# Optimization experiments

Hardware: AMD Instinct MI355X
Metric: run time of the kernel (lower is better)

The kernel has to match this reference:

```python
import jax, jax.numpy as jnp
import numpy as np

D_MODEL = 1024
K_QUERY = 32
K_TOPK = 4

def setup_inputs() -> dict:
    key = jax.random.key(0)
    k1, k2, k3, k4, k5 = jax.random.split(key, 5)
    x = jax.random.normal(k1, (4, 2048, D_MODEL), dtype=jnp.float32)
    # nn.Linear(d_model, k_query): weight [k_query, d_model], bias [k_query]
    sc = 1.0 / np.sqrt(D_MODEL)
    Wq = jax.random.uniform(k2, (K_QUERY, D_MODEL), jnp.float32, -sc, sc)
    bq = jax.random.uniform(k3, (K_QUERY,), jnp.float32, -sc, sc)
    Wk = jax.random.uniform(k4, (K_QUERY, D_MODEL), jnp.float32, -sc, sc)
    bk = jax.random.uniform(k5, (K_QUERY,), jnp.float32, -sc, sc)
    return {"x": x, "Wq": Wq, "bq": bq, "Wk": Wk, "bk": bk}

def reference(x, Wq, bq, Wk, bk):
    # x: [B, T, D]
    queries = jnp.einsum('btd,kd->btk', x, Wq) + bq      # [B, T, Kq]
    keys = jnp.einsum('btd,kd->btk', x, Wk) + bk         # [B, T, Kq]
    sim = jnp.einsum('btk,bsk->bts', queries, keys)      # [B, T, T]
    sim = sim / jnp.sqrt(jnp.float32(queries.shape[-1]))
    _, topk_idx = jax.lax.top_k(sim, K_TOPK)              # [B, T, K]
    # gather neighbors per (b, t): x[b, topk_idx[b, t]] -> [B, T, K, D]
    neighbors = jax.vmap(lambda xb, ib: xb[ib])(x, topk_idx)
    gathered = neighbors.mean(axis=2)                     # [B, T, D]
    return gathered
```

## Files before the change

kernel.cpp:

```cpp
#include <hip/hip_runtime.h>
#include <math.h>

#define D_MODEL 1024
#define T_SEQ   2048
#define NBATCH  4
#define NROWS   (NBATCH * T_SEQ)
#define NOUT    64
#define DCHUNK  256
#define NCHUNK  4

#define SKLD 264
#define SQLD 20

__device__ __forceinline__ bool key_gt(float av, int ai, float bv, int bi) {
    return (av > bv) || (av == bv && ai < bi);
}

__device__ __forceinline__ void cmpswap(float& v0, int& i0, float& v1, int& i1) {
    bool sw = key_gt(v1, i1, v0, i0);
    float nv0 = sw ? v1 : v0, nv1 = sw ? v0 : v1;
    int   ni0 = sw ? i1 : i0, ni1 = sw ? i0 : i1;
    v0 = nv0; v1 = nv1; i0 = ni0; i1 = ni1;
}

__device__ __forceinline__ void merge4(float (&a)[4], int (&ai)[4],
                                       float b0, int j0, float b1, int j1,
                                       float b2, int j2, float b3, int j3) {
    if (!key_gt(a[0], ai[0], b3, j3)) { a[0] = b3; ai[0] = j3; }
    if (!key_gt(a[1], ai[1], b2, j2)) { a[1] = b2; ai[1] = j2; }
    if (!key_gt(a[2], ai[2], b1, j1)) { a[2] = b1; ai[2] = j1; }
    if (!key_gt(a[3], ai[3], b0, j0)) { a[3] = b0; ai[3] = j0; }
    cmpswap(a[0], ai[0], a[2], ai[2]);
    cmpswap(a[1], ai[1], a[3], ai[3]);
    cmpswap(a[0], ai[0], a[1], ai[1]);
    cmpswap(a[2], ai[2], a[3], ai[3]);
}

__device__ __forceinline__ void insert4(float (&tv)[4], int (&tix)[4], float v, int idx) {
    if (v > tv[3]) {
        bool g0 = v > tv[0], g1 = v > tv[1], g2 = v > tv[2];
        float n0 = g0 ? v : tv[0];
        int   m0 = g0 ? idx : tix[0];
        float n1 = g1 ? (g0 ? tv[0] : v) : tv[1];
        int   m1 = g1 ? (g0 ? tix[0] : idx) : tix[1];
        float n2 = g2 ? (g1 ? tv[1] : v) : tv[2];
        int   m2 = g2 ? (g1 ? tix[1] : idx) : tix[2];
        float n3 = g2 ? tv[2] : v;
        int   m3 = g2 ? tix[2] : idx;
        tv[0] = n0; tv[1] = n1; tv[2] = n2; tv[3] = n3;
        tix[0] = m0; tix[1] = m1; tix[2] = m2; tix[3] = m3;
    }
}

__global__ __launch_bounds__(256) void wprep_kernel(
    const float* __restrict__ Wq, const float* __restrict__ Wk,
    double* __restrict__ Wdt)
{
    const int idx = blockIdx.x * 256 + threadIdx.x;
    const int o = idx & 63;
    const int d = idx >> 6;
    float v = (o < 32) ? Wq[(size_t)o * D_MODEL + d]
                       : Wk[(size_t)(o - 32) * D_MODEL + d];
    Wdt[(size_t)d * 64 + o] = (double)v;
}

__global__ __launch_bounds__(256) void proj_partial(
    const float* __restrict__ x, const double* __restrict__ Wdt,
    double* __restrict__ part )
{
    const int rl = threadIdx.x & 63;
    const int og = __builtin_amdgcn_readfirstlane(threadIdx.x >> 6);
    const int rb = blockIdx.x & 127;
    const int c  = blockIdx.x >> 7;
    const int row = rb * 64 + rl;
    const int d0  = c * DCHUNK;

    const float4* xr = reinterpret_cast<const float4*>(x + (size_t)row * D_MODEL + d0);
    const double* wbase = Wdt + (size_t)d0 * 64 + og * 16;

    double acc[16];
    #pragma unroll
    for (int j = 0; j < 16; ++j) acc[j] = 0.0;

    #pragma unroll 2
    for (int i = 0; i < DCHUNK / 4; ++i) {
        float4 xv = xr[i];
        double xd[4] = {xv.x, xv.y, xv.z, xv.w};
        #pragma unroll
        for (int u = 0; u < 4; ++u) {
            const double* w = wbase + (size_t)(i * 4 + u) * 64;
            #pragma unroll
            for (int j = 0; j < 16; ++j)
                acc[j] = fma(xd[u], w[j], acc[j]);
        }
    }

    double* p = part + ((size_t)c * NOUT + og * 16) * NROWS + row;
    #pragma unroll
    for (int j = 0; j < 16; ++j)
        p[(size_t)j * NROWS] = acc[j];
}

__global__ __launch_bounds__(256) void proj_combine(
    const double* __restrict__ part,
    const float* __restrict__ bq, const float* __restrict__ bk,
    float* __restrict__ Qt, float* __restrict__ Kt)
{
    const int idx = blockIdx.x * 256 + threadIdx.x;
    const int out = idx >> 13;
    const int row = idx & (NROWS - 1);
    double s = 0.0;
    #pragma unroll
    for (int c = 0; c < NCHUNK; ++c)
        s += part[((size_t)c * NOUT + out) * NROWS + row];
    const int b = row >> 11, t = row & 2047;
    if (out < 32) {
        Qt[((size_t)b * 32 + out) * T_SEQ + t] = (float)(s + (double)bq[out]);
    } else {
        Kt[((size_t)b * 32 + (out - 32)) * T_SEQ + t] = (float)(s + (double)bk[out - 32]);
    }
}

__global__ __launch_bounds__(256) void topk_gather_kernel(
    const float* __restrict__ x, const float* __restrict__ Qt,
    const float* __restrict__ Kt, float* __restrict__ out)
{
    __shared__ float klds[32 * SKLD];
    __shared__ float qlds[32 * SQLD];
    __shared__ float candV[4][16][4];
    __shared__ int   candI[4][16][4];
    __shared__ int   topIdx[16][4];

    const int tid  = threadIdx.x;
    const int lane = tid & 63;
    const int wav  = tid >> 6;
    const int b    = blockIdx.x >> 7;
    const int tblk = (blockIdx.x & 127) * 16;

    const float* QtB = Qt + (size_t)b * 32 * T_SEQ;
    const float* KtB = Kt + (size_t)b * 32 * T_SEQ;

    if (tid < 128) {
        const int i  = tid >> 2;
        const int t4 = (tid & 3) * 4;
        float4 v = *reinterpret_cast<const float4*>(QtB + (size_t)i * T_SEQ + tblk + t4);
        *reinterpret_cast<float4*>(&qlds[i * SQLD + t4]) = v;
    }

    const int tg = tid & 3;
    const int t0 = tg * 4;
    const int s0 = (tid >> 2) * 4;

    float tv[4][4]; int tix[4][4];
    #pragma unroll
    for (int r = 0; r < 4; ++r)
        #pragma unroll
        for (int j = 0; j < 4; ++j) { tv[r][j] = -INFINITY; tix[r][j] = 0x7fffffff; }

    for (int st = 0; st < 8; ++st) {
        __syncthreads();
        #pragma unroll
        for (int j = 0; j < 8; ++j) {
            const int f  = (tid + j * 256) * 4;
            const int ki = f >> 8;
            const int ks = f & 255;
            float4 v = *reinterpret_cast<const float4*>(KtB + (size_t)ki * T_SEQ + st * 256 + ks);
            *reinterpret_cast<float4*>(&klds[ki * SKLD + ks]) = v;
        }
        __syncthreads();

        float acc[4][4];
        #pragma unroll
        for (int r = 0; r < 4; ++r)
            #pragma unroll
            for (int c = 0; c < 4; ++c) acc[r][c] = 0.f;

        #pragma unroll 8
        for (int i = 0; i < 32; ++i) {
            float4 qv = *reinterpret_cast<const float4*>(&qlds[i * SQLD + t0]);
            float4 kv = *reinterpret_cast<const float4*>(&klds[i * SKLD + s0]);
            const float qa[4] = {qv.x, qv.y, qv.z, qv.w};
            const float ka[4] = {kv.x, kv.y, kv.z, kv.w};
            #pragma unroll
            for (int r = 0; r < 4; ++r)
                #pragma unroll
                for (int c = 0; c < 4; ++c)
                    acc[r][c] = fmaf(qa[r], ka[c], acc[r][c]);
        }

        const int sbase = st * 256 + s0;
        #pragma unroll
        for (int c = 0; c < 4; ++c)
            #pragma unroll
            for (int r = 0; r < 4; ++r)
                insert4(tv[r], tix[r], acc[r][c], sbase + c);
    }

    #pragma unroll
    for (int m = 4; m <= 32; m <<= 1) {
        #pragma unroll
        for (int r = 0; r < 4; ++r) {
            float b0 = __shfl_xor(tv[r][0], m, 64);
            float b1 = __shfl_xor(tv[r][1], m, 64);
            float b2 = __shfl_xor(tv[r][2], m, 64);
            float b3 = __shfl_xor(tv[r][3], m, 64);
            int   j0 = __shfl_xor(tix[r][0], m, 64);
            int   j1 = __shfl_xor(tix[r][1], m, 64);
            int   j2 = __shfl_xor(tix[r][2], m, 64);
            int   j3 = __shfl_xor(tix[r][3], m, 64);
            merge4(tv[r], tix[r], b0, j0, b1, j1, b2, j2, b3, j3);
        }
    }

    if (lane < 4) {
        #pragma unroll
        for (int r = 0; r < 4; ++r)
            #pragma unroll
            for (int j = 0; j < 4; ++j) {
                candV[wav][lane * 4 + r][j] = tv[r][j];
                candI[wav][lane * 4 + r][j] = tix[r][j];
            }
    }
    __syncthreads();

    if (tid < 16) {
        float mv[4]; int mi[4];
        #pragma unroll
        for (int j = 0; j < 4; ++j) { mv[j] = candV[0][tid][j]; mi[j] = candI[0][tid][j]; }
        #pragma unroll
        for (int w = 1; w < 4; ++w)
            merge4(mv, mi,
                   candV[w][tid][0], candI[w][tid][0],
                   candV[w][tid][1], candI[w][tid][1],
                   candV[w][tid][2], candI[w][tid][2],
                   candV[w][tid][3], candI[w][tid][3]);
        #pragma unroll
        for (int j = 0; j < 4; ++j) topIdx[tid][j] = mi[j];
    }
    __syncthreads();

    const float* xb = x + (size_t)b * T_SEQ * D_MODEL;
    float* ob = out + ((size_t)b * T_SEQ + tblk) * D_MODEL;
    for (int r = 0; r < 16; ++r) {
        const int i0 = topIdx[r][0], i1 = topIdx[r][1], i2 = topIdx[r][2], i3 = topIdx[r][3];
        float4 a0 = *(reinterpret_cast<const float4*>(xb + (size_t)i0 * D_MODEL) + tid);
        float4 a1 = *(reinterpret_cast<const float4*>(xb + (size_t)i1 * D_MODEL) + tid);
        float4 a2 = *(reinterpret_cast<const float4*>(xb + (size_t)i2 * D_MODEL) + tid);
        float4 a3 = *(reinterpret_cast<const float4*>(xb + (size_t)i3 * D_MODEL) + tid);
        float4 o;
        o.x = (a0.x + a1.x + a2.x + a3.x) * 0.25f;
        o.y = (a0.y + a1.y + a2.y + a3.y) * 0.25f;
        o.z = (a0.z + a1.z + a2.z + a3.z) * 0.25f;
        o.w = (a0.w + a1.w + a2.w + a3.w) * 0.25f;
        *(reinterpret_cast<float4*>(ob + (size_t)r * D_MODEL) + tid) = o;
    }
}

extern "C" void kernel_launch(void* const* d_in, const int* in_sizes, int n_in,
                              void* d_out, int out_size, void* d_ws, size_t ws_size,
                              hipStream_t stream) {
    const float* x  = (const float*)d_in[0];
    const float* Wq = (const float*)d_in[1];
    const float* bq = (const float*)d_in[2];
    const float* Wk = (const float*)d_in[3];
    const float* bk = (const float*)d_in[4];
    float* out = (float*)d_out;

    char* wsb = (char*)d_ws;
    double* Wdt  = (double*)wsb;
    float*  Qt   = (float*)(wsb + (size_t)D_MODEL * NOUT * 8);
    float*  Kt   = Qt + (size_t)NBATCH * 32 * T_SEQ;
    double* part = (double*)(wsb + (size_t)D_MODEL * NOUT * 8
                                 + 2 * (size_t)NBATCH * 32 * T_SEQ * 4);

    wprep_kernel<<<dim3(256), dim3(256), 0, stream>>>(Wq, Wk, Wdt);
    proj_partial<<<dim3(NCHUNK * 128), dim3(256), 0, stream>>>(x, Wdt, part);
    proj_combine<<<dim3(NOUT * NROWS / 256), dim3(256), 0, stream>>>(part, bq, bk, Qt, Kt);
    topk_gather_kernel<<<dim3(512), dim3(256), 0, stream>>>(x, Qt, Kt, out);
}
```

Baseline: 179.7 us.

## Split similarity top-k across key halves and separate gather into merge kernel

The fused top-k/gather kernel is split into two kernels. The first computes similarity and a partial top-4 over half of the key sequence per block, using 128 threads with 4x8 register tiles, which doubles the block count. The second merges the two partial candidate lists and gathers/averages rows of x, 8 rows per block. The projection kernel also now uses 512 threads, each computing 8 outputs instead of 16. This adds an extra launch and a global round trip for the candidates in exchange for more parallelism and lower register pressure.

```diff
diff --git a/kernel.cpp b/kernel.cpp
--- a/kernel.cpp
+++ b/kernel.cpp
@@ -64,7 +64,7 @@
     Wdt[(size_t)d * 64 + o] = (double)v;
 }
 
-__global__ __launch_bounds__(256) void proj_partial(
+__global__ __launch_bounds__(512) void proj_partial(
     const float* __restrict__ x, const double* __restrict__ Wdt,
     double* __restrict__ part )
 {
@@ -76,13 +76,13 @@
     const int d0  = c * DCHUNK;
 
     const float4* xr = reinterpret_cast<const float4*>(x + (size_t)row * D_MODEL + d0);
-    const double* wbase = Wdt + (size_t)d0 * 64 + og * 16;
-
-    double acc[16];
-    #pragma unroll
-    for (int j = 0; j < 16; ++j) acc[j] = 0.0;
-
-    #pragma unroll 2
+    const double* wbase = Wdt + (size_t)d0 * 64 + og * 8;
+
+    double acc[8];
+    #pragma unroll
+    for (int j = 0; j < 8; ++j) acc[j] = 0.0;
+
+    #pragma unroll 4
     for (int i = 0; i < DCHUNK / 4; ++i) {
         float4 xv = xr[i];
         double xd[4] = {xv.x, xv.y, xv.z, xv.w};
@@ -90,14 +90,14 @@
         for (int u = 0; u < 4; ++u) {
             const double* w = wbase + (size_t)(i * 4 + u) * 64;
             #pragma unroll
-            for (int j = 0; j < 16; ++j)
+            for (int j = 0; j < 8; ++j)
                 acc[j] = fma(xd[u], w[j], acc[j]);
         }
     }
 
-    double* p = part + ((size_t)c * NOUT + og * 16) * NROWS + row;
-    #pragma unroll
-    for (int j = 0; j < 16; ++j)
+    double* p = part + ((size_t)c * NOUT + og * 8) * NROWS + row;
+    #pragma unroll
+    for (int j = 0; j < 8; ++j)
         p[(size_t)j * NROWS] = acc[j];
 }
 
@@ -121,26 +121,29 @@
     }
 }
 
-__global__ __launch_bounds__(256) void topk_gather_kernel(
-    const float* __restrict__ x, const float* __restrict__ Qt,
-    const float* __restrict__ Kt, float* __restrict__ out)
+__global__ __launch_bounds__(128) void sim_topk(
+    const float* __restrict__ Qt, const float* __restrict__ Kt,
+    float* __restrict__ candVal ,
+    int*   __restrict__ candIdx )
 {
     __shared__ float klds[32 * SKLD];
     __shared__ float qlds[32 * SQLD];
-    __shared__ float candV[4][16][4];
-    __shared__ int   candI[4][16][4];
-    __shared__ int   topIdx[16][4];
+    __shared__ float cV[2][16][4];
+    __shared__ int   cI[2][16][4];
 
     const int tid  = threadIdx.x;
     const int lane = tid & 63;
     const int wav  = tid >> 6;
-    const int b    = blockIdx.x >> 7;
-    const int tblk = (blockIdx.x & 127) * 16;
+    const int half = blockIdx.x & 1;
+    const int tt   = (blockIdx.x >> 1) & 127;
+    const int b    = blockIdx.x >> 8;
+    const int tblk = tt * 16;
+    const int sh0  = half * 1024;
 
     const float* QtB = Qt + (size_t)b * 32 * T_SEQ;
     const float* KtB = Kt + (size_t)b * 32 * T_SEQ;
 
-    if (tid < 128) {
+    {
         const int i  = tid >> 2;
         const int t4 = (tid & 3) * 4;
         float4 v = *reinterpret_cast<const float4*>(QtB + (size_t)i * T_SEQ + tblk + t4);
@@ -149,7 +152,7 @@
 
     const int tg = tid & 3;
     const int t0 = tg * 4;
-    const int s0 = (tid >> 2) * 4;
+    const int s0 = (tid >> 2) * 8;
 
     float tv[4][4]; int tix[4][4];
     #pragma unroll
@@ -157,40 +160,42 @@
         #pragma unroll
         for (int j = 0; j < 4; ++j) { tv[r][j] = -INFINITY; tix[r][j] = 0x7fffffff; }
 
-    for (int st = 0; st < 8; ++st) {
+    for (int st = 0; st < 4; ++st) {
         __syncthreads();
         #pragma unroll
-        for (int j = 0; j < 8; ++j) {
-            const int f  = (tid + j * 256) * 4;
+        for (int j = 0; j < 16; ++j) {
+            const int f  = (tid + j * 128) * 4;
             const int ki = f >> 8;
             const int ks = f & 255;
-            float4 v = *reinterpret_cast<const float4*>(KtB + (size_t)ki * T_SEQ + st * 256 + ks);
+            float4 v = *reinterpret_cast<const float4*>(
+                KtB + (size_t)ki * T_SEQ + sh0 + st * 256 + ks);
             *reinterpret_cast<float4*>(&klds[ki * SKLD + ks]) = v;
         }
         __syncthreads();
 
-        float acc[4][4];
+        float acc[4][8];
         #pragma unroll
         for (int r = 0; r < 4; ++r)
             #pragma unroll
-            for (int c = 0; c < 4; ++c) acc[r][c] = 0.f;
-
-        #pragma unroll 8
+            for (int c = 0; c < 8; ++c) acc[r][c] = 0.f;
+
+        #pragma unroll 4
         for (int i = 0; i < 32; ++i) {
-            float4 qv = *reinterpret_cast<const float4*>(&qlds[i * SQLD + t0]);
-            float4 kv = *reinterpret_cast<const float4*>(&klds[i * SKLD + s0]);
+            float4 qv  = *reinterpret_cast<const float4*>(&qlds[i * SQLD + t0]);
+            float4 kv0 = *reinterpret_cast<const float4*>(&klds[i * SKLD + s0]);
+            float4 kv1 = *reinterpret_cast<const float4*>(&klds[i * SKLD + s0 + 4]);
             const float qa[4] = {qv.x, qv.y, qv.z, qv.w};
-            const float ka[4] = {kv.x, kv.y, kv.z, kv.w};
+            const float ka[8] = {kv0.x, kv0.y, kv0.z, kv0.w, kv1.x, kv1.y, kv1.z, kv1.w};
             #pragma unroll
             for (int r = 0; r < 4; ++r)
                 #pragma unroll
-                for (int c = 0; c < 4; ++c)
+                for (int c = 0; c < 8; ++c)
                     acc[r][c] = fmaf(qa[r], ka[c], acc[r][c]);
         }
 
-        const int sbase = st * 256 + s0;
-        #pragma unroll
-        for (int c = 0; c < 4; ++c)
+        const int sbase = sh0 + st * 256 + s0;
+        #pragma unroll
+        for (int c = 0; c < 8; ++c)
             #pragma unroll
             for (int r = 0; r < 4; ++r)
                 insert4(tv[r], tix[r], acc[r][c], sbase + c);
@@ -217,8 +222,8 @@
         for (int r = 0; r < 4; ++r)
             #pragma unroll
             for (int j = 0; j < 4; ++j) {
-                candV[wav][lane * 4 + r][j] = tv[r][j];
-                candI[wav][lane * 4 + r][j] = tix[r][j];
+                cV[wav][lane * 4 + r][j] = tv[r][j];
+                cI[wav][lane * 4 + r][j] = tix[r][j];
             }
     }
     __syncthreads();
@@ -226,22 +231,49 @@
     if (tid < 16) {
         float mv[4]; int mi[4];
         #pragma unroll
-        for (int j = 0; j < 4; ++j) { mv[j] = candV[0][tid][j]; mi[j] = candI[0][tid][j]; }
-        #pragma unroll
-        for (int w = 1; w < 4; ++w)
-            merge4(mv, mi,
-                   candV[w][tid][0], candI[w][tid][0],
-                   candV[w][tid][1], candI[w][tid][1],
-                   candV[w][tid][2], candI[w][tid][2],
-                   candV[w][tid][3], candI[w][tid][3]);
+        for (int j = 0; j < 4; ++j) { mv[j] = cV[0][tid][j]; mi[j] = cI[0][tid][j]; }
+        merge4(mv, mi,
+               cV[1][tid][0], cI[1][tid][0],
+               cV[1][tid][1], cI[1][tid][1],
+               cV[1][tid][2], cI[1][tid][2],
+               cV[1][tid][3], cI[1][tid][3]);
+        const size_t row = (size_t)b * T_SEQ + tblk + tid;
+        float4 vv = {mv[0], mv[1], mv[2], mv[3]};
+        int4   ii = {mi[0], mi[1], mi[2], mi[3]};
+        *reinterpret_cast<float4*>(candVal + ((size_t)half * NROWS + row) * 4) = vv;
+        *reinterpret_cast<int4*>(candIdx + ((size_t)half * NROWS + row) * 4) = ii;
+    }
+}
+
+__global__ __launch_bounds__(256) void merge_gather(
+    const float* __restrict__ x,
+    const float* __restrict__ candVal, const int* __restrict__ candIdx,
+    float* __restrict__ out)
+{
+    __shared__ int topIdx[8][4];
+
+    const int tid  = threadIdx.x;
+    const int row0 = blockIdx.x * 8;
+    const int b    = row0 >> 11;
+
+    if (tid < 8) {
+        const size_t row = row0 + tid;
+        float4 v0 = *reinterpret_cast<const float4*>(candVal + row * 4);
+        int4   i0 = *reinterpret_cast<const int4*>(candIdx + row * 4);
+        float4 v1 = *reinterpret_cast<const float4*>(candVal + ((size_t)NROWS + row) * 4);
+        int4   i1 = *reinterpret_cast<const int4*>(candIdx + ((size_t)NROWS + row) * 4);
+        float mv[4] = {v0.x, v0.y, v0.z, v0.w};
+        int   mi[4] = {i0.x, i0.y, i0.z, i0.w};
+        merge4(mv, mi, v1.x, i1.x, v1.y, i1.y, v1.z, i1.z, v1.w, i1.w);
         #pragma unroll
         for (int j = 0; j < 4; ++j) topIdx[tid][j] = mi[j];
     }
     __syncthreads();
 
     const float* xb = x + (size_t)b * T_SEQ * D_MODEL;
-    float* ob = out + ((size_t)b * T_SEQ + tblk) * D_MODEL;
-    for (int r = 0; r < 16; ++r) {
+    float* ob = out + (size_t)row0 * D_MODEL;
+    #pragma unroll
+    for (int r = 0; r < 8; ++r) {
         const int i0 = topIdx[r][0], i1 = topIdx[r][1], i2 = topIdx[r][2], i3 = topIdx[r][3];
         float4 a0 = *(reinterpret_cast<const float4*>(xb + (size_t)i0 * D_MODEL) + tid);
         float4 a1 = *(reinterpret_cast<const float4*>(xb + (size_t)i1 * D_MODEL) + tid);
@@ -272,9 +304,12 @@
     float*  Kt   = Qt + (size_t)NBATCH * 32 * T_SEQ;
     double* part = (double*)(wsb + (size_t)D_MODEL * NOUT * 8
                                  + 2 * (size_t)NBATCH * 32 * T_SEQ * 4);
+    float*  candVal = (float*)((char*)part + (size_t)NCHUNK * NOUT * NROWS * 8);
+    int*    candIdx = (int*)((char*)candVal + (size_t)2 * NROWS * 4 * 4);
 
     wprep_kernel<<<dim3(256), dim3(256), 0, stream>>>(Wq, Wk, Wdt);
-    proj_partial<<<dim3(NCHUNK * 128), dim3(256), 0, stream>>>(x, Wdt, part);
+    proj_partial<<<dim3(NCHUNK * 128), dim3(512), 0, stream>>>(x, Wdt, part);
     proj_combine<<<dim3(NOUT * NROWS / 256), dim3(256), 0, stream>>>(part, bq, bk, Qt, Kt);
-    topk_gather_kernel<<<dim3(512), dim3(256), 0, stream>>>(x, Qt, Kt, out);
-}
+    sim_topk<<<dim3(1024), dim3(128), 0, stream>>>(Qt, Kt, candVal, candIdx);
+    merge_gather<<<dim3(1024), dim3(256), 0, stream>>>(x, candVal, candIdx, out);
+}
```

New measurement: 173.8 us. 1.03x faster.
